# Kernel optimization log

Measured on AMD Instinct MI355X. Metric: run time of the kernel, lower is better.

Reference implementation:

```python
import jax, jax.numpy as jnp
import numpy as np

B, S, E, H = 2, 2048, 2048, 16
HD = E // H  # head_dim = 128


def _rope(x):
    # x: (B, S, H, HD). Faithful to source: sin/cos built from head_dim,
    # but _rotate_every_two operates on the SEQUENCE axis (axis 1) and the
    # rearrange 'b d j ... -> b (d j) ...' with d=2 concatenates, not interleaves.
    s, hd = x.shape[1], x.shape[-1]
    inv_freq = 1.0 / 10000 ** (np.arange(0, hd, 2) / hd)          # (hd/2,)
    sinusoid = np.einsum('i,j->ij', np.arange(s), inv_freq)       # (s, hd/2)
    # einops.repeat 'b n -> b (n j)', j=2 interleaves each element twice
    sin = np.repeat(np.sin(sinusoid), 2, axis=1)[-s:, None, :]    # (s, 1, hd)
    cos = np.repeat(np.cos(sinusoid), 2, axis=1)[-s:, None, :]
    sin = jnp.asarray(sin, x.dtype)
    cos = jnp.asarray(cos, x.dtype)
    odds = x[:, 1::2]   # (B, S/2, H, HD)
    evens = x[:, ::2]
    rot = jnp.concatenate([-odds, evens], axis=1)  # (B, S, H, HD)
    return x * cos + rot * sin


def setup_inputs() -> dict:
    key = jax.random.key(0)
    k_in, kq, kk, kv, ko = jax.random.split(key, 5)
    scale_in = (1.0 / E) ** 0.5   # lecun_normal fan_in = E
    scale_out = (1.0 / E) ** 0.5  # out_proj fan_in = H*HD = E
    return {
        'inputs': jax.random.normal(k_in, (B, S, E), dtype=jnp.float32),
        'mask': jnp.zeros((1, 1, S, S), dtype=jnp.float32),
        'wq': jax.random.normal(kq, (E, H, HD), dtype=jnp.float32) * scale_in,
        'wk': jax.random.normal(kk, (E, H, HD), dtype=jnp.float32) * scale_in,
        'wv': jax.random.normal(kv, (E, H, HD), dtype=jnp.float32) * scale_in,
        'wo': jax.random.normal(ko, (H, HD, E), dtype=jnp.float32) * scale_out,
        'train': 0,
    }


def reference(inputs, mask, wq, wk, wv, wo, train):
    # QKV projections: (B,S,E) x (E,H,HD) -> (B,S,H,HD)
    q = jnp.einsum('bse,ehd->bshd', inputs, wq)
    k = jnp.einsum('bse,ehd->bshd', inputs, wk)
    v = jnp.einsum('bse,ehd->bshd', inputs, wv)
    q = _rope(q)
    k = _rope(k)
    # scores + custom norm: x / (2*hidden_dim)**(-0.5) == x * sqrt(2*E)
    norm_scale = (2.0 * E) ** 0.5
    qk = jnp.einsum('bshe,bShe->bhsS', q, k)
    attn = jax.nn.softmax((qk + mask) * norm_scale, axis=-1)
    self_attn = jnp.einsum('bhsS,bShe->bshe', attn, v)  # (B,S,H,HD)
    # out projection contracts (heads, kv): (B,S,H,HD) x (H,HD,E) -> (B,S,E)
    return jnp.einsum('bshd,hde->bse', self_attn, wo)
```

## Files before the change

### kernel.cpp

```cpp
#include <hip/hip_runtime.h>
#include <hip/hip_bf16.h>
#include <cmath>

#define Bn 2
#define Sn 2048
#define En 2048
#define Hn 16
#define HDn 128
#define Mn (Bn*Sn)
#define NORMS2 92.33248261689366f

typedef __attribute__((ext_vector_type(8))) short short8;
typedef __attribute__((ext_vector_type(4))) float f32x4;

__device__ __forceinline__ short f2bf(float x) {
    __hip_bfloat16 h = __float2bfloat16(x);
    return *reinterpret_cast<short*>(&h);
}
__device__ __forceinline__ float bf2f(short s) {
    __hip_bfloat16 h = *reinterpret_cast<__hip_bfloat16*>(&s);
    return __bfloat162float(h);
}
__device__ __forceinline__ void gl_lds16(const void* g, void* l) {
    __builtin_amdgcn_global_load_lds(
        (const __attribute__((address_space(1))) unsigned int*)g,
        (__attribute__((address_space(3))) unsigned int*)l, 16, 0, 0);
}

#if __has_builtin(__builtin_amdgcn_exp2f)
#define EXP2(x) __builtin_amdgcn_exp2f(x)
#else
#define EXP2(x) exp2f(x)
#endif

template<int CTRL>
__device__ __forceinline__ float dppf(float x) {
    int r = __builtin_amdgcn_update_dpp(0, __builtin_bit_cast(int, x), CTRL, 0xf, 0xf, true);
    return __builtin_bit_cast(float, r);
}
__device__ __forceinline__ float redmax16(float x) {
    x = fmaxf(x, dppf<0xB1>(x));
    x = fmaxf(x, dppf<0x4E>(x));
    x = fmaxf(x, dppf<0x141>(x));
    x = fmaxf(x, dppf<0x140>(x));
    return x;
}
__device__ __forceinline__ float redsum16(float x) {
    x += dppf<0xB1>(x);
    x += dppf<0x4E>(x);
    x += dppf<0x141>(x);
    x += dppf<0x140>(x);
    return x;
}

static __global__ void rope_table_kernel(float* __restrict__ sinT, float* __restrict__ cosT) {
    int i = blockIdx.x * 256 + threadIdx.x;
    int t = i >> 6, f = i & 63;
    double inv = pow(10000.0, -(double)(2 * f) / (double)HDn);
    double ang = (double)t * inv;
    sinT[i] = (float)sin(ang);
    cosT[i] = (float)cos(ang);
}

static __global__ void split_x_kernel(const float* __restrict__ X,
                                      short* __restrict__ Xhi, short* __restrict__ Xlo) {
    int i = (blockIdx.x * 256 + threadIdx.x) * 4;
    float4 x = *(const float4*)&X[i];
    short4 hi, lo;
    hi.x = f2bf(x.x); lo.x = f2bf(x.x - bf2f(hi.x));
    hi.y = f2bf(x.y); lo.y = f2bf(x.y - bf2f(hi.y));
    hi.z = f2bf(x.z); lo.z = f2bf(x.z - bf2f(hi.z));
    hi.w = f2bf(x.w); lo.w = f2bf(x.w - bf2f(hi.w));
    *(short4*)&Xhi[i] = hi;
    *(short4*)&Xlo[i] = lo;
}

static __global__ void maskconv_kernel(const float* __restrict__ M, short* __restrict__ MB) {
    int i = (blockIdx.x * 256 + threadIdx.x) * 4;
    float4 m = *(const float4*)&M[i];
    short4 o;
    o.x = f2bf(m.x * NORMS2); o.y = f2bf(m.y * NORMS2);
    o.z = f2bf(m.z * NORMS2); o.w = f2bf(m.w * NORMS2);
    *(short4*)&MB[i] = o;
}

static __global__ __launch_bounds__(256) void wtrans4_kernel(
        const float* __restrict__ Wq, const float* __restrict__ Wk,
        const float* __restrict__ Wv, const float* __restrict__ Wo,
        short* __restrict__ QKh, short* __restrict__ QKl,
        short* __restrict__ VT, short* __restrict__ OT) {
    __shared__ float tile[32][33];
    const int z = blockIdx.z;
    const float* W = (z == 0) ? Wq : (z == 1) ? Wk : (z == 2) ? Wv : Wo;
    short* Th = (z <= 1) ? QKh : (z == 2) ? VT : OT;
    const int rowoff = (z == 1) ? 2048 : 0;
    const bool split = (z <= 1);
    int tx = threadIdx.x & 31, ty = threadIdx.x >> 5;
    int k0 = blockIdx.y * 32, n0 = blockIdx.x * 32;
    #pragma unroll
    for (int i = 0; i < 4; ++i)
        tile[ty + i * 8][tx] = W[(size_t)(k0 + ty + i * 8) * En + n0 + tx];
    __syncthreads();
    #pragma unroll
    for (int i = 0; i < 4; ++i) {
        float v = tile[tx][ty + i * 8];
        size_t idx = (size_t)(rowoff + n0 + ty + i * 8) * En + k0 + tx;
        short hv = f2bf(v);
        Th[idx] = hv;
        if (split) QKl[idx] = f2bf(v - bf2f(hv));
    }
}

template<int NPROD, int OUTMODE>
static __global__ __launch_bounds__(256) void gemm_kernel(
        const short* __restrict__ Ahi, const short* __restrict__ Alo,
        const short* __restrict__ Bhi, const short* __restrict__ Blo,
        float* __restrict__ Cf, short* __restrict__ Cbt,
        int* __restrict__ Qpk, int* __restrict__ Kpk) {
    __shared__ short As_hi[128 * 32];
    __shared__ short Bs_hi[128 * 32];
    __shared__ short As_lo[NPROD == 3 ? 128 * 32 : 8];
    __shared__ short Bs_lo[NPROD == 3 ? 128 * 32 : 8];
    __shared__ short Ts[OUTMODE == 1 ? 128 * 136 : 8];

    const int tid = threadIdx.x;
    const int w = tid >> 6, l = tid & 63;
    const int quad = l >> 4, l15 = l & 15;
    const int wr = (w >> 1) * 64, wc = (w & 1) * 64;
    const int row0 = blockIdx.y * 128, col0 = blockIdx.x * 128;

    const int off0 = tid * 16;
    const int r_a = off0 >> 6;
    const int kb = (off0 & 63) >> 1;

    f32x4 acc[4][4];
    #pragma unroll
    for (int i = 0; i < 4; ++i)
        #pragma unroll
        for (int j = 0; j < 4; ++j) acc[i][j] = f32x4{0.f, 0.f, 0.f, 0.f};

    for (int k0 = 0; k0 < En; k0 += 32) {
        const short* ap = Ahi + (size_t)(row0 + r_a) * En + k0 + kb;
        const short* bp = Bhi + (size_t)(col0 + r_a) * En + k0 + kb;
        gl_lds16(ap,           &As_hi[off0 / 2]);
        gl_lds16(ap + 64 * En, &As_hi[(off0 + 4096) / 2]);
        gl_lds16(bp,           &Bs_hi[off0 / 2]);
        gl_lds16(bp + 64 * En, &Bs_hi[(off0 + 4096) / 2]);
        if constexpr (NPROD == 3) {
            const short* ap2 = Alo + (size_t)(row0 + r_a) * En + k0 + kb;
            const short* bp2 = Blo + (size_t)(col0 + r_a) * En + k0 + kb;
            gl_lds16(ap2,           &As_lo[off0 / 2]);
            gl_lds16(ap2 + 64 * En, &As_lo[(off0 + 4096) / 2]);
            gl_lds16(bp2,           &Bs_lo[off0 / 2]);
            gl_lds16(bp2 + 64 * En, &Bs_lo[(off0 + 4096) / 2]);
        }
        __syncthreads();

        short8 bhf[4], blf[4];
        #pragma unroll
        for (int ni = 0; ni < 4; ++ni) {
            bhf[ni] = *(const short8*)&Bs_hi[(wc + ni * 16 + l15) * 32 + quad * 8];
            if constexpr (NPROD == 3)
                blf[ni] = *(const short8*)&Bs_lo[(wc + ni * 16 + l15) * 32 + quad * 8];
        }
        #pragma unroll
        for (int mi = 0; mi < 4; ++mi) {
            short8 ahf = *(const short8*)&As_hi[(wr + mi * 16 + l15) * 32 + quad * 8];
            short8 alf;
            if constexpr (NPROD == 3)
                alf = *(const short8*)&As_lo[(wr + mi * 16 + l15) * 32 + quad * 8];
            #pragma unroll
            for (int ni = 0; ni < 4; ++ni) {
                acc[mi][ni] = __builtin_amdgcn_mfma_f32_16x16x32_bf16(ahf, bhf[ni], acc[mi][ni], 0, 0, 0);
                if constexpr (NPROD == 3) {
                    acc[mi][ni] = __builtin_amdgcn_mfma_f32_16x16x32_bf16(ahf, blf[ni], acc[mi][ni], 0, 0, 0);
                    acc[mi][ni] = __builtin_amdgcn_mfma_f32_16x16x32_bf16(alf, bhf[ni], acc[mi][ni], 0, 0, 0);
                }
            }
        }
        __syncthreads();
    }

    if constexpr (OUTMODE == 0) {
        #pragma unroll
        for (int mi = 0; mi < 4; ++mi)
            #pragma unroll
            for (int ni = 0; ni < 4; ++ni) {
                int r = row0 + wr + mi * 16 + quad * 4;
                int c = col0 + wc + ni * 16 + l15;
                #pragma unroll
                for (int reg = 0; reg < 4; ++reg)
                    Cf[(size_t)(r + reg) * En + c] = acc[mi][ni][reg];
            }
    } else if constexpr (OUTMODE == 1) {
        #pragma unroll
        for (int mi = 0; mi < 4; ++mi)
            #pragma unroll
            for (int ni = 0; ni < 4; ++ni) {
                int dl = wc + ni * 16 + l15;
                int sl = wr + mi * 16 + quad * 4;
                #pragma unroll
                for (int reg = 0; reg < 4; ++reg)
                    Ts[dl * 136 + sl + reg] = f2bf(acc[mi][ni][reg]);
            }
        __syncthreads();
        int dl = tid >> 1, s0 = (tid & 1) * 64;
        int b = row0 >> 11, h = col0 >> 7;
        size_t gbase = ((size_t)(b * Hn + h) * HDn + dl) * Sn + (row0 & (Sn - 1)) + s0;
        #pragma unroll
        for (int k = 0; k < 8; ++k) {
            short8 vv = *(const short8*)&Ts[dl * 136 + s0 + k * 8];
            *(short8*)&Cbt[gbase + k * 8] = vv;
        }
    } else {
        int* dst = (col0 >= 2048) ? Kpk : Qpk;
        const int cb = col0 & 2047;
        #pragma unroll
        for (int mi = 0; mi < 4; ++mi)
            #pragma unroll
            for (int ni = 0; ni < 4; ++ni) {
                int r = row0 + wr + mi * 16 + quad * 4;
                int c = cb + wc + ni * 16 + l15;
                #pragma unroll
                for (int reg = 0; reg < 4; ++reg) {
                    float v = acc[mi][ni][reg];
                    short hh = f2bf(v);
                    short ll = f2bf(v - bf2f(hh));
                    dst[(size_t)(r + reg) * 2048 + c] =
                        ((int)(unsigned short)hh << 16) | (unsigned short)ll;
                }
            }
    }
}

static __global__ void rope_pk_kernel(const int* __restrict__ Pre,
        short* __restrict__ Yh, short* __restrict__ Yl,
        const float* __restrict__ sinT, const float* __restrict__ cosT) {
    int p = blockIdx.x * 256 + threadIdx.x;
    int u = p & 511;
    int t = (p >> 9) & (Sn - 1);
    int b = p >> 20;
    int tsrc; float sgn;
    if (t < Sn / 2) { tsrc = 2 * t + 1; sgn = -1.f; }
    else            { tsrc = 2 * (t - Sn / 2); sgn = 1.f; }
    int f0 = (2 * u) & 63, f1 = (2 * u + 1) & 63;
    float sv0 = sinT[(t << 6) + f0], cv0 = cosT[(t << 6) + f0];
    float sv1 = sinT[(t << 6) + f1], cv1 = cosT[(t << 6) + f1];
    size_t rt = ((size_t)(b * Sn + t)) * 512 + u;
    size_t rs = ((size_t)(b * Sn + tsrc)) * 512 + u;
    int4 xt = ((const int4*)Pre)[rt];
    int4 xs = ((const int4*)Pre)[rs];
    auto up = [](int v) -> float {
        return bf2f((short)(v >> 16)) + bf2f((short)(v & 0xffff));
    };
    float x0 = up(xt.x), x1 = up(xt.y), x2 = up(xt.z), x3 = up(xt.w);
    float s0 = up(xs.x), s1 = up(xs.y), s2 = up(xs.z), s3 = up(xs.w);
    float y0 = x0 * cv0 + sgn * s0 * sv0;
    float y1 = x1 * cv0 + sgn * s1 * sv0;
    float y2 = x2 * cv1 + sgn * s2 * sv1;
    float y3 = x3 * cv1 + sgn * s3 * sv1;
    short4 hi, lo;
    hi.x = f2bf(y0); lo.x = f2bf(y0 - bf2f(hi.x));
    hi.y = f2bf(y1); lo.y = f2bf(y1 - bf2f(hi.y));
    hi.z = f2bf(y2); lo.z = f2bf(y2 - bf2f(hi.z));
    hi.w = f2bf(y3); lo.w = f2bf(y3 - bf2f(hi.w));
    size_t o = ((size_t)(b * Sn + t)) * En + 4 * u;
    *(short4*)&Yh[o] = hi;
    *(short4*)&Yl[o] = lo;
}

static __global__ __launch_bounds__(512, 2) void flash5_kernel(
        const short* __restrict__ Qhi, const short* __restrict__ Qlo,
        const short* __restrict__ Khi, const short* __restrict__ Klo,
        const short* __restrict__ Vt, const short* __restrict__ maskB,
        short* __restrict__ AO) {
    __shared__ short lds0[34816];

    const int tid = threadIdx.x;
    const int w = tid >> 6, l = tid & 63;
    const int quad = l >> 4, l15 = l & 15;
    const int n = blockIdx.x;
    const int bh = (n & 7) * 4 + ((n >> 3) & 3);
    const int qt = n >> 5;
    const int b = bh >> 4, h = bh & 15;
    const int r0 = qt * 128;
    const size_t qkbase = (size_t)b * Sn * En + (size_t)h * HDn;
    const int psb = 24576 + w * 1280;

    #pragma unroll
    for (int c = 0; c < 4; ++c) {
        int off = tid * 16 + c * 8192;
        int row = off >> 8;
        int gp = (off >> 4) & 15;
        int gl = gp ^ (row & 7);
        size_t gidx = qkbase + (size_t)(r0 + row) * En + gl * 8;
        gl_lds16(Qhi + gidx, &lds0[off / 2]);
        gl_lds16(Qlo + gidx, &lds0[16384 + off / 2]);
    }
    __syncthreads();
    short8 qh[4], ql[4];
    {
        int row = 16 * w + l15;
        #pragma unroll
        for (int kc = 0; kc < 4; ++kc) {
            int gp = (kc * 4 + quad) ^ (row & 7);
            qh[kc] = *(const short8*)&lds0[row * 128 + gp * 8];
            ql[kc] = *(const short8*)&lds0[16384 + row * 128 + gp * 8];
        }
    }

    f32x4 O[8];
    #pragma unroll
    for (int di = 0; di < 8; ++di) O[di] = f32x4{0.f, 0.f, 0.f, 0.f};
    float m_prev[4] = {-INFINITY, -INFINITY, -INFINITY, -INFINITY};
    float l_run[4] = {0.f, 0.f, 0.f, 0.f};
    const int qrow_base = r0 + 16 * w + quad * 4;

    for (int j0 = 0; j0 < Sn; j0 += 64) {
        __syncthreads();
        #pragma unroll
        for (int c = 0; c < 2; ++c) {
            int off = tid * 16 + c * 8192;
            int row = off >> 8;
            int gp = (off >> 4) & 15;
            int gl = gp ^ (row & 7);
            size_t gidx = qkbase + (size_t)(j0 + row) * En + gl * 8;
            gl_lds16(Khi + gidx, &lds0[off / 2]);
            gl_lds16(Klo + gidx, &lds0[8192 + off / 2]);
        }
        #pragma unroll
        for (int c = 0; c < 2; ++c) {
            int off = tid * 16 + c * 8192;
            int vrow = off >> 7;
            int vgp = (off >> 4) & 7;
            int vgl = vgp ^ (vrow & 7);
            size_t vidx = ((size_t)bh * HDn + vrow) * Sn + j0 + vgl * 8;
            gl_lds16(Vt + vidx, &lds0[16384 + off / 2]);
        }
        float mv[4][4];
        #pragma unroll
        for (int ni = 0; ni < 4; ++ni)
            #pragma unroll
            for (int reg = 0; reg < 4; ++reg)
                mv[ni][reg] = bf2f(maskB[(size_t)(qrow_base + reg) * Sn + j0 + ni * 16 + l15]);
        __syncthreads();

        f32x4 p[4];
        #pragma unroll
        for (int ni = 0; ni < 4; ++ni) p[ni] = f32x4{0.f, 0.f, 0.f, 0.f};
        #pragma unroll
        for (int ni = 0; ni < 4; ++ni) {
            int col = ni * 16 + l15;
            #pragma unroll
            for (int kc = 0; kc < 4; ++kc) {
                int gp = (kc * 4 + quad) ^ (col & 7);
                short8 kh = *(const short8*)&lds0[col * 128 + gp * 8];
                short8 kl = *(const short8*)&lds0[8192 + col * 128 + gp * 8];
                p[ni] = __builtin_amdgcn_mfma_f32_16x16x32_bf16(qh[kc], kh, p[ni], 0, 0, 0);
                p[ni] = __builtin_amdgcn_mfma_f32_16x16x32_bf16(qh[kc], kl, p[ni], 0, 0, 0);
                p[ni] = __builtin_amdgcn_mfma_f32_16x16x32_bf16(ql[kc], kh, p[ni], 0, 0, 0);
            }
        }

        float rm[4] = {-INFINITY, -INFINITY, -INFINITY, -INFINITY};
        #pragma unroll
        for (int ni = 0; ni < 4; ++ni)
            #pragma unroll
            for (int reg = 0; reg < 4; ++reg) {
                float v = fmaf(p[ni][reg], NORMS2, mv[ni][reg]);
                p[ni][reg] = v;
                rm[reg] = fmaxf(rm[reg], v);
            }
        #pragma unroll
        for (int reg = 0; reg < 4; ++reg) rm[reg] = redmax16(rm[reg]);
        float al[4], mn[4], rs[4];
        #pragma unroll
        for (int reg = 0; reg < 4; ++reg) {
            mn[reg] = fmaxf(m_prev[reg], rm[reg]);
            al[reg] = EXP2(m_prev[reg] - mn[reg]);
            rs[reg] = 0.f;
        }
        #pragma unroll
        for (int ni = 0; ni < 4; ++ni)
            #pragma unroll
            for (int reg = 0; reg < 4; ++reg) {
                float pe = EXP2(p[ni][reg] - mn[reg]);
                rs[reg] += pe;
                lds0[psb + (quad * 4 + reg) * 80 + ((ni ^ quad) << 4) + l15] = f2bf(pe);
            }
        #pragma unroll
        for (int reg = 0; reg < 4; ++reg) rs[reg] = redsum16(rs[reg]);
        #pragma unroll
        for (int reg = 0; reg < 4; ++reg) {
            l_run[reg] = l_run[reg] * al[reg] + rs[reg];
            m_prev[reg] = mn[reg];
        }
        #pragma unroll
        for (int di = 0; di < 8; ++di)
            #pragma unroll
            for (int reg = 0; reg < 4; ++reg)
                O[di][reg] *= al[reg];

        short8 pa[2];
        #pragma unroll
        for (int kc2 = 0; kc2 < 2; ++kc2) {
            int g = kc2 * 2 + (quad >> 1);
            int gs = g ^ (l15 >> 2);
            pa[kc2] = *(const short8*)&lds0[psb + l15 * 80 + (gs << 4) + (quad & 1) * 8];
        }

        #pragma unroll
        for (int di = 0; di < 8; ++di) {
            int d = di * 16 + l15;
            #pragma unroll
            for (int kc2 = 0; kc2 < 2; ++kc2) {
                int gp = (kc2 * 4 + quad) ^ (d & 7);
                short8 vb = *(const short8*)&lds0[16384 + d * 64 + gp * 8];
                O[di] = __builtin_amdgcn_mfma_f32_16x16x32_bf16(pa[kc2], vb, O[di], 0, 0, 0);
            }
        }
    }

    float inv[4];
    #pragma unroll
    for (int reg = 0; reg < 4; ++reg) inv[reg] = 1.0f / l_run[reg];
    #pragma unroll
    for (int di = 0; di < 8; ++di)
        #pragma unroll
        for (int reg = 0; reg < 4; ++reg) {
            size_t idx = ((size_t)b * Sn + qrow_base + reg) * En + h * HDn + di * 16 + l15;
            AO[idx] = f2bf(O[di][reg] * inv[reg]);
        }
}

extern "C" void kernel_launch(void* const* d_in, const int* in_sizes, int n_in,
                              void* d_out, int out_size, void* d_ws, size_t ws_size,
                              hipStream_t stream) {
    const float* inputs = (const float*)d_in[0];
    const float* mask   = (const float*)d_in[1];
    const float* wq     = (const float*)d_in[2];
    const float* wk     = (const float*)d_in[3];
    const float* wv     = (const float*)d_in[4];
    const float* wo     = (const float*)d_in[5];
    float* out = (float*)d_out;
    (void)in_sizes; (void)n_in; (void)out_size; (void)ws_size;

    char* W8 = (char*)d_ws;
    float* sinT  = (float*)(W8 + 0);
    float* cosT  = (float*)(W8 + 524288);
    short* Xhi   = (short*)(W8 + 1048576);
    short* Xlo   = (short*)(W8 + 17825792);
    short* maskB = (short*)(W8 + 34603008);
    short* WqkTh = (short*)(W8 + 42991616);
    short* WqkTl = (short*)(W8 + 59768832);
    short* WvT   = (short*)(W8 + 76546048);
    short* WoT   = (short*)(W8 + 84934656);
    int*   Qpk   = (int*)(W8 + 93323264);
    int*   Kpk   = (int*)(W8 + 126877696);
    short* Qhi = WqkTh;
    short* Qlo = WqkTl;
    short* Khi = (short*)(W8 + 93323264);
    short* Klo = (short*)(W8 + 110100480);
    short* Vt  = (short*)(W8 + 126877696);
    short* AO  = Xhi;

    rope_table_kernel<<<512, 256, 0, stream>>>(sinT, cosT);
    split_x_kernel<<<8192, 256, 0, stream>>>(inputs, Xhi, Xlo);
    maskconv_kernel<<<4096, 256, 0, stream>>>(mask, maskB);
    wtrans4_kernel<<<dim3(64, 64, 4), 256, 0, stream>>>(wq, wk, wv, wo,
                                                        WqkTh, WqkTl, WvT, WoT);

    gemm_kernel<3, 3><<<dim3(32, 32), 256, 0, stream>>>(
        Xhi, Xlo, WqkTh, WqkTl, nullptr, nullptr, Qpk, Kpk);
    rope_pk_kernel<<<8192, 256, 0, stream>>>(Qpk, Qhi, Qlo, sinT, cosT);
    rope_pk_kernel<<<8192, 256, 0, stream>>>(Kpk, Khi, Klo, sinT, cosT);
    gemm_kernel<1, 1><<<dim3(16, 32), 256, 0, stream>>>(
        Xhi, nullptr, WvT, nullptr, nullptr, Vt, nullptr, nullptr);

    flash5_kernel<<<512, 512, 0, stream>>>(Qhi, Qlo, Khi, Klo, Vt, maskB, AO);

    gemm_kernel<1, 0><<<dim3(16, 32), 256, 0, stream>>>(
        AO, nullptr, WoT, nullptr, out, nullptr, nullptr, nullptr);
}
```

Baseline: 695.2 us.

## Register-prefetch K/V tiles, lazy softmax rescale, and MFMA priority in flash kernel

Replaces the direct global-to-LDS loads of K/V with register prefetch of the next tile, issued during the current tile's compute and stored to LDS at the top of the next iteration. Softmax rescaling of O and l is skipped unless some row max grows by more than a threshold of 8 (wave-uniform check), which cuts per-tile multiplies. s_setprio is raised around the MFMA loops, and launch bounds are raised to 4 blocks per CU. This risks register pressure or spills from the extra prefetch registers combined with the tighter launch bound. Lazy rescaling can also let exp2 values exceed 1, up to 2^8, which slightly changes numerics.

```diff
diff --git a/kernel.cpp b/kernel.cpp
--- a/kernel.cpp
+++ b/kernel.cpp
@@ -269,7 +269,7 @@
     *(short4*)&Yl[o] = lo;
 }
 
-static __global__ __launch_bounds__(512, 2) void flash5_kernel(
+static __global__ __launch_bounds__(512, 4) void flash6_kernel(
         const short* __restrict__ Qhi, const short* __restrict__ Qlo,
         const short* __restrict__ Khi, const short* __restrict__ Klo,
         const short* __restrict__ Vt, const short* __restrict__ maskB,
@@ -297,6 +297,20 @@
         gl_lds16(Qhi + gidx, &lds0[off / 2]);
         gl_lds16(Qlo + gidx, &lds0[16384 + off / 2]);
     }
+
+    const int offA = tid * 16, offB = offA + 8192;
+    const int krA = offA >> 8, krB = offB >> 8;
+    const size_t kgA = qkbase + (size_t)krA * En + ((((offA >> 4) & 15) ^ (krA & 7)) << 3);
+    const size_t kgB = qkbase + (size_t)krB * En + ((((offB >> 4) & 15) ^ (krB & 7)) << 3);
+    const int vrA = offA >> 7, vrB = offB >> 7;
+    const size_t vgA = ((size_t)bh * HDn + vrA) * Sn + ((((offA >> 4) & 7) ^ (vrA & 7)) << 3);
+    const size_t vgB = ((size_t)bh * HDn + vrB) * Sn + ((((offB >> 4) & 7) ^ (vrB & 7)) << 3);
+
+    int4 sKh0, sKh1, sKl0, sKl1, sV0, sV1;
+    sKh0 = *(const int4*)(Khi + kgA); sKl0 = *(const int4*)(Klo + kgA);
+    sKh1 = *(const int4*)(Khi + kgB); sKl1 = *(const int4*)(Klo + kgB);
+    sV0  = *(const int4*)(Vt + vgA);  sV1  = *(const int4*)(Vt + vgB);
+
     __syncthreads();
     short8 qh[4], ql[4];
     {
@@ -318,36 +332,33 @@
 
     for (int j0 = 0; j0 < Sn; j0 += 64) {
         __syncthreads();
-        #pragma unroll
-        for (int c = 0; c < 2; ++c) {
-            int off = tid * 16 + c * 8192;
-            int row = off >> 8;
-            int gp = (off >> 4) & 15;
-            int gl = gp ^ (row & 7);
-            size_t gidx = qkbase + (size_t)(j0 + row) * En + gl * 8;
-            gl_lds16(Khi + gidx, &lds0[off / 2]);
-            gl_lds16(Klo + gidx, &lds0[8192 + off / 2]);
-        }
-        #pragma unroll
-        for (int c = 0; c < 2; ++c) {
-            int off = tid * 16 + c * 8192;
-            int vrow = off >> 7;
-            int vgp = (off >> 4) & 7;
-            int vgl = vgp ^ (vrow & 7);
-            size_t vidx = ((size_t)bh * HDn + vrow) * Sn + j0 + vgl * 8;
-            gl_lds16(Vt + vidx, &lds0[16384 + off / 2]);
-        }
+        *(int4*)&lds0[offA / 2]         = sKh0;
+        *(int4*)&lds0[offB / 2]         = sKh1;
+        *(int4*)&lds0[8192 + offA / 2]  = sKl0;
+        *(int4*)&lds0[8192 + offB / 2]  = sKl1;
+        *(int4*)&lds0[16384 + offA / 2] = sV0;
+        *(int4*)&lds0[16384 + offB / 2] = sV1;
+        __syncthreads();
+
         float mv[4][4];
         #pragma unroll
         for (int ni = 0; ni < 4; ++ni)
             #pragma unroll
             for (int reg = 0; reg < 4; ++reg)
                 mv[ni][reg] = bf2f(maskB[(size_t)(qrow_base + reg) * Sn + j0 + ni * 16 + l15]);
-        __syncthreads();
+
+        if (j0 + 64 < Sn) {
+            const size_t kd = (size_t)(j0 + 64) * En;
+            sKh0 = *(const int4*)(Khi + kgA + kd); sKl0 = *(const int4*)(Klo + kgA + kd);
+            sKh1 = *(const int4*)(Khi + kgB + kd); sKl1 = *(const int4*)(Klo + kgB + kd);
+            sV0  = *(const int4*)(Vt + vgA + (j0 + 64));
+            sV1  = *(const int4*)(Vt + vgB + (j0 + 64));
+        }
 
         f32x4 p[4];
         #pragma unroll
         for (int ni = 0; ni < 4; ++ni) p[ni] = f32x4{0.f, 0.f, 0.f, 0.f};
+        __builtin_amdgcn_s_setprio(1);
         #pragma unroll
         for (int ni = 0; ni < 4; ++ni) {
             int col = ni * 16 + l15;
@@ -361,6 +372,7 @@
                 p[ni] = __builtin_amdgcn_mfma_f32_16x16x32_bf16(ql[kc], kh, p[ni], 0, 0, 0);
             }
         }
+        __builtin_amdgcn_s_setprio(0);
 
         float rm[4] = {-INFINITY, -INFINITY, -INFINITY, -INFINITY};
         #pragma unroll
@@ -373,33 +385,32 @@
             }
         #pragma unroll
         for (int reg = 0; reg < 4; ++reg) rm[reg] = redmax16(rm[reg]);
-        float al[4], mn[4], rs[4];
-        #pragma unroll
-        for (int reg = 0; reg < 4; ++reg) {
-            mn[reg] = fmaxf(m_prev[reg], rm[reg]);
-            al[reg] = EXP2(m_prev[reg] - mn[reg]);
-            rs[reg] = 0.f;
-        }
+        bool grow = (rm[0] > m_prev[0] + 8.f) || (rm[1] > m_prev[1] + 8.f)
+                 || (rm[2] > m_prev[2] + 8.f) || (rm[3] > m_prev[3] + 8.f);
+        if (__any((int)grow)) {
+            #pragma unroll
+            for (int reg = 0; reg < 4; ++reg) {
+                float mn = fmaxf(m_prev[reg], rm[reg]);
+                float al = EXP2(m_prev[reg] - mn);
+                m_prev[reg] = mn;
+                l_run[reg] *= al;
+                #pragma unroll
+                for (int di = 0; di < 8; ++di) O[di][reg] *= al;
+            }
+        }
+        float rs[4] = {0.f, 0.f, 0.f, 0.f};
         #pragma unroll
         for (int ni = 0; ni < 4; ++ni)
             #pragma unroll
             for (int reg = 0; reg < 4; ++reg) {
-                float pe = EXP2(p[ni][reg] - mn[reg]);
+                float pe = EXP2(p[ni][reg] - m_prev[reg]);
                 rs[reg] += pe;
                 lds0[psb + (quad * 4 + reg) * 80 + ((ni ^ quad) << 4) + l15] = f2bf(pe);
             }
         #pragma unroll
         for (int reg = 0; reg < 4; ++reg) rs[reg] = redsum16(rs[reg]);
         #pragma unroll
-        for (int reg = 0; reg < 4; ++reg) {
-            l_run[reg] = l_run[reg] * al[reg] + rs[reg];
-            m_prev[reg] = mn[reg];
-        }
-        #pragma unroll
-        for (int di = 0; di < 8; ++di)
-            #pragma unroll
-            for (int reg = 0; reg < 4; ++reg)
-                O[di][reg] *= al[reg];
+        for (int reg = 0; reg < 4; ++reg) l_run[reg] += rs[reg];
 
         short8 pa[2];
         #pragma unroll
@@ -409,6 +420,7 @@
             pa[kc2] = *(const short8*)&lds0[psb + l15 * 80 + (gs << 4) + (quad & 1) * 8];
         }
 
+        __builtin_amdgcn_s_setprio(1);
         #pragma unroll
         for (int di = 0; di < 8; ++di) {
             int d = di * 16 + l15;
@@ -419,6 +431,7 @@
                 O[di] = __builtin_amdgcn_mfma_f32_16x16x32_bf16(pa[kc2], vb, O[di], 0, 0, 0);
             }
         }
+        __builtin_amdgcn_s_setprio(0);
     }
 
     float inv[4];
@@ -477,7 +490,7 @@
     gemm_kernel<1, 1><<<dim3(16, 32), 256, 0, stream>>>(
         Xhi, nullptr, WvT, nullptr, nullptr, Vt, nullptr, nullptr);
 
-    flash5_kernel<<<512, 512, 0, stream>>>(Qhi, Qlo, Khi, Klo, Vt, maskB, AO);
+    flash6_kernel<<<512, 512, 0, stream>>>(Qhi, Qlo, Khi, Klo, Vt, maskB, AO);
 
     gemm_kernel<1, 0><<<dim3(16, 32), 256, 0, stream>>>(
         AO, nullptr, WoT, nullptr, out, nullptr, nullptr, nullptr);
```

Measured after the change: 848.8 us. +22.1%, slower.

## Process two 16-row query tiles per wave in flash attention with 256-thread blocks

Applied to the files above, without the earlier changes.

The flash attention kernel now runs 4 waves per block instead of 8, and each wave handles 32 query rows (two 16-row subtiles) instead of 16. Each K/V fragment read from LDS is reused across both subtiles, which halves K and V LDS traffic per MFMA, and the tile loads are spread over fewer threads. The cost is roughly double the accumulator and Q-fragment registers per wave, which may lower occupancy or cause spills, and fewer waves are available to hide latency.

```diff
diff --git a/kernel.cpp b/kernel.cpp
--- a/kernel.cpp
+++ b/kernel.cpp
@@ -269,7 +269,7 @@
     *(short4*)&Yl[o] = lo;
 }
 
-static __global__ __launch_bounds__(512, 2) void flash5_kernel(
+static __global__ __launch_bounds__(256, 2) void flash8_kernel(
         const short* __restrict__ Qhi, const short* __restrict__ Qlo,
         const short* __restrict__ Khi, const short* __restrict__ Klo,
         const short* __restrict__ Vt, const short* __restrict__ maskB,
@@ -285,11 +285,11 @@
     const int b = bh >> 4, h = bh & 15;
     const int r0 = qt * 128;
     const size_t qkbase = (size_t)b * Sn * En + (size_t)h * HDn;
-    const int psb = 24576 + w * 1280;
-
-    #pragma unroll
-    for (int c = 0; c < 4; ++c) {
-        int off = tid * 16 + c * 8192;
+    const int psb = 24576 + w * 2560;
+
+    #pragma unroll
+    for (int c = 0; c < 8; ++c) {
+        int off = tid * 16 + c * 4096;
         int row = off >> 8;
         int gp = (off >> 4) & 15;
         int gl = gp ^ (row & 7);
@@ -298,29 +298,35 @@
         gl_lds16(Qlo + gidx, &lds0[16384 + off / 2]);
     }
     __syncthreads();
-    short8 qh[4], ql[4];
-    {
-        int row = 16 * w + l15;
+    short8 qh[2][4], ql[2][4];
+    #pragma unroll
+    for (int rh = 0; rh < 2; ++rh) {
+        int row = 32 * w + 16 * rh + l15;
         #pragma unroll
         for (int kc = 0; kc < 4; ++kc) {
             int gp = (kc * 4 + quad) ^ (row & 7);
-            qh[kc] = *(const short8*)&lds0[row * 128 + gp * 8];
-            ql[kc] = *(const short8*)&lds0[16384 + row * 128 + gp * 8];
-        }
-    }
-
-    f32x4 O[8];
-    #pragma unroll
-    for (int di = 0; di < 8; ++di) O[di] = f32x4{0.f, 0.f, 0.f, 0.f};
-    float m_prev[4] = {-INFINITY, -INFINITY, -INFINITY, -INFINITY};
-    float l_run[4] = {0.f, 0.f, 0.f, 0.f};
-    const int qrow_base = r0 + 16 * w + quad * 4;
+            qh[rh][kc] = *(const short8*)&lds0[row * 128 + gp * 8];
+            ql[rh][kc] = *(const short8*)&lds0[16384 + row * 128 + gp * 8];
+        }
+    }
+
+    f32x4 O[2][8];
+    #pragma unroll
+    for (int rh = 0; rh < 2; ++rh)
+        #pragma unroll
+        for (int di = 0; di < 8; ++di) O[rh][di] = f32x4{0.f, 0.f, 0.f, 0.f};
+    float m_prev[2][4], l_run[2][4];
+    #pragma unroll
+    for (int rh = 0; rh < 2; ++rh)
+        #pragma unroll
+        for (int reg = 0; reg < 4; ++reg) { m_prev[rh][reg] = -INFINITY; l_run[rh][reg] = 0.f; }
+    const int qrow_base = r0 + 32 * w + quad * 4;
 
     for (int j0 = 0; j0 < Sn; j0 += 64) {
         __syncthreads();
         #pragma unroll
-        for (int c = 0; c < 2; ++c) {
-            int off = tid * 16 + c * 8192;
+        for (int c = 0; c < 4; ++c) {
+            int off = tid * 16 + c * 4096;
             int row = off >> 8;
             int gp = (off >> 4) & 15;
             int gl = gp ^ (row & 7);
@@ -329,25 +335,29 @@
             gl_lds16(Klo + gidx, &lds0[8192 + off / 2]);
         }
         #pragma unroll
-        for (int c = 0; c < 2; ++c) {
-            int off = tid * 16 + c * 8192;
+        for (int c = 0; c < 4; ++c) {
+            int off = tid * 16 + c * 4096;
             int vrow = off >> 7;
             int vgp = (off >> 4) & 7;
             int vgl = vgp ^ (vrow & 7);
             size_t vidx = ((size_t)bh * HDn + vrow) * Sn + j0 + vgl * 8;
             gl_lds16(Vt + vidx, &lds0[16384 + off / 2]);
         }
-        float mv[4][4];
-        #pragma unroll
-        for (int ni = 0; ni < 4; ++ni)
-            #pragma unroll
-            for (int reg = 0; reg < 4; ++reg)
-                mv[ni][reg] = bf2f(maskB[(size_t)(qrow_base + reg) * Sn + j0 + ni * 16 + l15]);
+        float mv[2][4][4];
+        #pragma unroll
+        for (int rh = 0; rh < 2; ++rh)
+            #pragma unroll
+            for (int ni = 0; ni < 4; ++ni)
+                #pragma unroll
+                for (int reg = 0; reg < 4; ++reg)
+                    mv[rh][ni][reg] = bf2f(maskB[(size_t)(qrow_base + 16 * rh + reg) * Sn + j0 + ni * 16 + l15]);
         __syncthreads();
 
-        f32x4 p[4];
-        #pragma unroll
-        for (int ni = 0; ni < 4; ++ni) p[ni] = f32x4{0.f, 0.f, 0.f, 0.f};
+        f32x4 p[2][4];
+        #pragma unroll
+        for (int rh = 0; rh < 2; ++rh)
+            #pragma unroll
+            for (int ni = 0; ni < 4; ++ni) p[rh][ni] = f32x4{0.f, 0.f, 0.f, 0.f};
         #pragma unroll
         for (int ni = 0; ni < 4; ++ni) {
             int col = ni * 16 + l15;
@@ -356,58 +366,66 @@
                 int gp = (kc * 4 + quad) ^ (col & 7);
                 short8 kh = *(const short8*)&lds0[col * 128 + gp * 8];
                 short8 kl = *(const short8*)&lds0[8192 + col * 128 + gp * 8];
-                p[ni] = __builtin_amdgcn_mfma_f32_16x16x32_bf16(qh[kc], kh, p[ni], 0, 0, 0);
-                p[ni] = __builtin_amdgcn_mfma_f32_16x16x32_bf16(qh[kc], kl, p[ni], 0, 0, 0);
-                p[ni] = __builtin_amdgcn_mfma_f32_16x16x32_bf16(ql[kc], kh, p[ni], 0, 0, 0);
-            }
-        }
-
-        float rm[4] = {-INFINITY, -INFINITY, -INFINITY, -INFINITY};
-        #pragma unroll
-        for (int ni = 0; ni < 4; ++ni)
+                #pragma unroll
+                for (int rh = 0; rh < 2; ++rh) {
+                    p[rh][ni] = __builtin_amdgcn_mfma_f32_16x16x32_bf16(qh[rh][kc], kh, p[rh][ni], 0, 0, 0);
+                    p[rh][ni] = __builtin_amdgcn_mfma_f32_16x16x32_bf16(qh[rh][kc], kl, p[rh][ni], 0, 0, 0);
+                    p[rh][ni] = __builtin_amdgcn_mfma_f32_16x16x32_bf16(ql[rh][kc], kh, p[rh][ni], 0, 0, 0);
+                }
+            }
+        }
+
+        #pragma unroll
+        for (int rh = 0; rh < 2; ++rh) {
+            float rm[4] = {-INFINITY, -INFINITY, -INFINITY, -INFINITY};
+            #pragma unroll
+            for (int ni = 0; ni < 4; ++ni)
+                #pragma unroll
+                for (int reg = 0; reg < 4; ++reg) {
+                    float v = fmaf(p[rh][ni][reg], NORMS2, mv[rh][ni][reg]);
+                    p[rh][ni][reg] = v;
+                    rm[reg] = fmaxf(rm[reg], v);
+                }
+            #pragma unroll
+            for (int reg = 0; reg < 4; ++reg) rm[reg] = redmax16(rm[reg]);
+            float al[4], mn[4], rs[4];
             #pragma unroll
             for (int reg = 0; reg < 4; ++reg) {
-                float v = fmaf(p[ni][reg], NORMS2, mv[ni][reg]);
-                p[ni][reg] = v;
-                rm[reg] = fmaxf(rm[reg], v);
-            }
-        #pragma unroll
-        for (int reg = 0; reg < 4; ++reg) rm[reg] = redmax16(rm[reg]);
-        float al[4], mn[4], rs[4];
-        #pragma unroll
-        for (int reg = 0; reg < 4; ++reg) {
-            mn[reg] = fmaxf(m_prev[reg], rm[reg]);
-            al[reg] = EXP2(m_prev[reg] - mn[reg]);
-            rs[reg] = 0.f;
-        }
-        #pragma unroll
-        for (int ni = 0; ni < 4; ++ni)
+                mn[reg] = fmaxf(m_prev[rh][reg], rm[reg]);
+                al[reg] = EXP2(m_prev[rh][reg] - mn[reg]);
+                rs[reg] = 0.f;
+            }
+            #pragma unroll
+            for (int ni = 0; ni < 4; ++ni)
+                #pragma unroll
+                for (int reg = 0; reg < 4; ++reg) {
+                    float pe = EXP2(p[rh][ni][reg] - mn[reg]);
+                    rs[reg] += pe;
+                    lds0[psb + (rh * 16 + quad * 4 + reg) * 80 + ((ni ^ quad) << 4) + l15] = f2bf(pe);
+                }
+            #pragma unroll
+            for (int reg = 0; reg < 4; ++reg) rs[reg] = redsum16(rs[reg]);
             #pragma unroll
             for (int reg = 0; reg < 4; ++reg) {
-                float pe = EXP2(p[ni][reg] - mn[reg]);
-                rs[reg] += pe;
-                lds0[psb + (quad * 4 + reg) * 80 + ((ni ^ quad) << 4) + l15] = f2bf(pe);
-            }
-        #pragma unroll
-        for (int reg = 0; reg < 4; ++reg) rs[reg] = redsum16(rs[reg]);
-        #pragma unroll
-        for (int reg = 0; reg < 4; ++reg) {
-            l_run[reg] = l_run[reg] * al[reg] + rs[reg];
-            m_prev[reg] = mn[reg];
-        }
-        #pragma unroll
-        for (int di = 0; di < 8; ++di)
-            #pragma unroll
-            for (int reg = 0; reg < 4; ++reg)
-                O[di][reg] *= al[reg];
-
-        short8 pa[2];
-        #pragma unroll
-        for (int kc2 = 0; kc2 < 2; ++kc2) {
-            int g = kc2 * 2 + (quad >> 1);
-            int gs = g ^ (l15 >> 2);
-            pa[kc2] = *(const short8*)&lds0[psb + l15 * 80 + (gs << 4) + (quad & 1) * 8];
-        }
+                l_run[rh][reg] = l_run[rh][reg] * al[reg] + rs[reg];
+                m_prev[rh][reg] = mn[reg];
+            }
+            #pragma unroll
+            for (int di = 0; di < 8; ++di)
+                #pragma unroll
+                for (int reg = 0; reg < 4; ++reg)
+                    O[rh][di][reg] *= al[reg];
+        }
+
+        short8 pa[2][2];
+        #pragma unroll
+        for (int rh = 0; rh < 2; ++rh)
+            #pragma unroll
+            for (int kc2 = 0; kc2 < 2; ++kc2) {
+                int g = kc2 * 2 + (quad >> 1);
+                int gs = g ^ (l15 >> 2);
+                pa[rh][kc2] = *(const short8*)&lds0[psb + (rh * 16 + l15) * 80 + (gs << 4) + (quad & 1) * 8];
+            }
 
         #pragma unroll
         for (int di = 0; di < 8; ++di) {
@@ -416,21 +434,26 @@
             for (int kc2 = 0; kc2 < 2; ++kc2) {
                 int gp = (kc2 * 4 + quad) ^ (d & 7);
                 short8 vb = *(const short8*)&lds0[16384 + d * 64 + gp * 8];
-                O[di] = __builtin_amdgcn_mfma_f32_16x16x32_bf16(pa[kc2], vb, O[di], 0, 0, 0);
-            }
-        }
-    }
-
-    float inv[4];
-    #pragma unroll
-    for (int reg = 0; reg < 4; ++reg) inv[reg] = 1.0f / l_run[reg];
-    #pragma unroll
-    for (int di = 0; di < 8; ++di)
-        #pragma unroll
-        for (int reg = 0; reg < 4; ++reg) {
-            size_t idx = ((size_t)b * Sn + qrow_base + reg) * En + h * HDn + di * 16 + l15;
-            AO[idx] = f2bf(O[di][reg] * inv[reg]);
-        }
+                #pragma unroll
+                for (int rh = 0; rh < 2; ++rh)
+                    O[rh][di] = __builtin_amdgcn_mfma_f32_16x16x32_bf16(pa[rh][kc2], vb, O[rh][di], 0, 0, 0);
+            }
+        }
+    }
+
+    #pragma unroll
+    for (int rh = 0; rh < 2; ++rh) {
+        float inv[4];
+        #pragma unroll
+        for (int reg = 0; reg < 4; ++reg) inv[reg] = 1.0f / l_run[rh][reg];
+        #pragma unroll
+        for (int di = 0; di < 8; ++di)
+            #pragma unroll
+            for (int reg = 0; reg < 4; ++reg) {
+                size_t idx = ((size_t)b * Sn + qrow_base + 16 * rh + reg) * En + h * HDn + di * 16 + l15;
+                AO[idx] = f2bf(O[rh][di][reg] * inv[reg]);
+            }
+    }
 }
 
 extern "C" void kernel_launch(void* const* d_in, const int* in_sizes, int n_in,
@@ -477,7 +500,7 @@
     gemm_kernel<1, 1><<<dim3(16, 32), 256, 0, stream>>>(
         Xhi, nullptr, WvT, nullptr, nullptr, Vt, nullptr, nullptr);
 
-    flash5_kernel<<<512, 512, 0, stream>>>(Qhi, Qlo, Khi, Klo, Vt, maskB, AO);
+    flash8_kernel<<<512, 256, 0, stream>>>(Qhi, Qlo, Khi, Klo, Vt, maskB, AO);
 
     gemm_kernel<1, 0><<<dim3(16, 32), 256, 0, stream>>>(
         AO, nullptr, WoT, nullptr, out, nullptr, nullptr, nullptr);
```

Measured after the change: 750.4 us. 7.9% more time.
